# Kernel optimization log

Measured on AMD Instinct MI355X. Metric: run time of the kernel, lower is better.

## Reference

```python
import jax, jax.numpy as jnp
import numpy as np

B, T, C = 2, 2048, 1024
H = 16
HS = C // H  # head_size = 64


def setup_inputs() -> dict:
    key = jax.random.key(0)
    k1, k2, k3 = jax.random.split(key, 3)
    x = jax.random.normal(k1, (B, T, C), dtype=jnp.float32)
    # nn.Linear(n_embd, 3*n_embd): weight [3C, C], bias [3C]
    W = jax.random.normal(k2, (3 * C, C), dtype=jnp.float32) * (C ** -0.5)
    b = jax.random.normal(k3, (3 * C,), dtype=jnp.float32) * 0.02
    return {"x": x, "W": W, "b": b}


def reference(x, W, b):
    Bs, Ts, Cs = x.shape
    # fused QKV projection: [B,T,3C]
    qkv = x @ W.T + b
    qkv = qkv.reshape(Bs, Ts, 3, H, HS)
    q, k, v = jnp.moveaxis(qkv, 2, 0)          # each [B,T,H,HS]
    q = q.transpose(0, 2, 1, 3)                 # [B,H,T,HS]
    k = k.transpose(0, 2, 1, 3)
    v = v.transpose(0, 2, 1, 3)
    scale = HS ** -0.5
    wei = jnp.einsum('bhqd,bhkd->bhqk', q, k) * scale  # [B,H,T,T]
    causal = jnp.tril(jnp.ones((Ts, Ts), dtype=bool))
    wei = jnp.where(causal, wei, -jnp.inf)
    wei = jax.nn.softmax(wei, axis=-1)
    out = jnp.einsum('bhqk,bhkd->bhqd', wei, v)        # [B,H,T,HS]
    return out.transpose(0, 2, 1, 3).reshape(Bs, Ts, Cs)
```

## Files before the change

### kernel.cpp

```cpp
#include <hip/hip_runtime.h>
#include <hip/hip_bf16.h>

typedef __attribute__((ext_vector_type(8))) short bf16x8;
typedef __attribute__((ext_vector_type(4))) float f32x4;

#define BATCH 2
#define T_SEQ 2048
#define C_EMB 1024
#define NH 16
#define HS 64

__device__ __forceinline__ void gld_lds16(const __hip_bfloat16* g, void* l) {
    __builtin_amdgcn_global_load_lds((const __attribute__((address_space(1))) uint32_t*)g,
                                     (__attribute__((address_space(3))) uint32_t*)l, 16, 0, 0);
}

__device__ __forceinline__ unsigned pk_bf16(float a, float b) {
    unsigned r;
    asm("v_cvt_pk_bf16_f32 %0, %1, %2" : "=v"(r) : "v"(a), "v"(b));
    return r;
}

__device__ __forceinline__ void pack_store(char* dst, float4 a, float4 b) {
    uint4 u;
    u.x = pk_bf16(a.x, a.y);
    u.y = pk_bf16(a.z, a.w);
    u.z = pk_bf16(b.x, b.y);
    u.w = pk_bf16(b.z, b.w);
    *(uint4*)dst = u;
}

#define NT_K 16

__launch_bounds__(512, 2)
__global__ void qkv_gemm(const float* __restrict__ xf,
                         const float* __restrict__ wf,
                         const float* __restrict__ bias,
                         __hip_bfloat16* __restrict__ qo,
                         __hip_bfloat16* __restrict__ ko,
                         __hip_bfloat16* __restrict__ vto)
{
    __shared__ __align__(16) char smem[114688];
    __hip_bfloat16* ASB = (__hip_bfloat16*)smem;
    __hip_bfloat16* BSB = (__hip_bfloat16*)(smem + 65536);
    const int nTn = (3 * C_EMB) / 192;
    int bid = blockIdx.x;
    int wgid = (bid & 7) * 32 + (bid >> 3);
    int bm = wgid / nTn, bn = wgid % nTn;
    int m0 = bm * 256, n0 = bn * 192;
    int tid  = threadIdx.x;
    int lane = tid & 63, w = tid >> 6;
    int wr = w >> 2, wc = w & 3;
    int c = lane & 15, g = lane >> 4;
    int sr = lane >> 2;
    int j  = lane & 3;
    int pc = j ^ ((sr >> 1) & 3);
    int rchnk = (g ^ ((c >> 1) & 3)) << 4;

#define LOAD_AB(kt, kh, pa_, pb_) { \
    int col_ = (kt) * 64 + (kh) * 32 + j * 8; \
    _Pragma("unroll") for (int i_ = 0; i_ < 2; ++i_) { \
        const float* s_ = &xf[(size_t)(m0 + w * 32 + i_ * 16 + sr) * 1024 + col_]; \
        pa_[2 * i_] = *(const float4*)s_; pa_[2 * i_ + 1] = *(const float4*)(s_ + 4); } \
    if (w < 4) { \
        _Pragma("unroll") for (int i_ = 0; i_ < 2; ++i_) { \
            const float* s_ = &wf[(size_t)(n0 + w * 32 + i_ * 16 + sr) * 1024 + col_]; \
            pb_[2 * i_] = *(const float4*)s_; pb_[2 * i_ + 1] = *(const float4*)(s_ + 4); } \
    } else { \
        const float* s_ = &wf[(size_t)(n0 + 128 + (w - 4) * 16 + sr) * 1024 + col_]; \
        pb_[0] = *(const float4*)s_; pb_[1] = *(const float4*)(s_ + 4); } }

#define WRITE_AB(tb_, pa_, pb_) { \
    _Pragma("unroll") for (int i_ = 0; i_ < 2; ++i_) \
        pack_store((char*)&ASB[(tb_) * 8192 + (w * 32 + i_ * 16 + sr) * 32 + pc * 8], \
                   pa_[2 * i_], pa_[2 * i_ + 1]); \
    if (w < 4) { \
        _Pragma("unroll") for (int i_ = 0; i_ < 2; ++i_) \
            pack_store((char*)&BSB[(tb_) * 6144 + (w * 32 + i_ * 16 + sr) * 32 + pc * 8], \
                       pb_[2 * i_], pb_[2 * i_ + 1]); \
    } else { \
        pack_store((char*)&BSB[(tb_) * 6144 + (128 + (w - 4) * 16 + sr) * 32 + pc * 8], \
                   pb_[0], pb_[1]); } }

    f32x4 acc[8][3];
#pragma unroll
    for (int mi = 0; mi < 8; ++mi)
#pragma unroll
        for (int ni = 0; ni < 3; ++ni)
            acc[mi][ni] = (f32x4){0.f, 0.f, 0.f, 0.f};

    float4 s0a[4], s0b[4], s1a[4], s1b[4];
    int tb_s0 = 0, tb_s1 = 0;
    bool v_s0 = false, v_s1 = false;

    LOAD_AB(0, 0, s0a, s0b); WRITE_AB(0, s0a, s0b);
    LOAD_AB(0, 1, s0a, s0b); WRITE_AB(1, s0a, s0b);
    LOAD_AB(1, 0, s1a, s1b); tb_s1 = 2; v_s1 = true;
    __syncthreads();

    for (int t = 0; t < NT_K; ++t) {
        int buf = t & 1;
#pragma unroll
        for (int ks = 0; ks < 2; ++ks) {
            const __hip_bfloat16* AL = &ASB[(buf * 2 + ks) * 8192];
            const __hip_bfloat16* BL = &BSB[(buf * 2 + ks) * 6144];
            bf16x8 bfr[3], af[8];
#pragma unroll
            for (int ni = 0; ni < 3; ++ni)
                bfr[ni] = *(const bf16x8*)((const char*)BL + (wc * 48 + ni * 16 + c) * 64 + rchnk);
#pragma unroll
            for (int mi = 0; mi < 8; ++mi)
                af[mi] = *(const bf16x8*)((const char*)AL + (wr * 128 + mi * 16 + c) * 64 + rchnk);
            if (ks == 0) {
                if (t + 1 < NT_K) { LOAD_AB(t + 1, 1, s0a, s0b); tb_s0 = ((t + 1) & 1) * 2 + 1; v_s0 = true; }
                else v_s0 = false;
            } else {
                if (t + 2 < NT_K) { LOAD_AB(t + 2, 0, s1a, s1b); tb_s1 = ((t + 2) & 1) * 2; v_s1 = true; }
                else v_s1 = false;
            }
            __builtin_amdgcn_s_setprio(1);
#pragma unroll
            for (int mi = 0; mi < 8; ++mi)
#pragma unroll
                for (int ni = 0; ni < 3; ++ni)
                    acc[mi][ni] = __builtin_amdgcn_mfma_f32_16x16x32_bf16(af[mi], bfr[ni], acc[mi][ni], 0, 0, 0);
            __builtin_amdgcn_s_setprio(0);
            if (ks == 0) { if (v_s1) WRITE_AB(tb_s1, s1a, s1b); }
            else         { if (v_s0) WRITE_AB(tb_s0, s0a, s0b); }
            asm volatile("s_waitcnt lgkmcnt(0)" ::: "memory");
            __builtin_amdgcn_s_barrier();
        }
    }
#undef LOAD_AB
#undef WRITE_AB

    const float QSCALE = 0.125f * 1.44269504088896340736f;
    __syncthreads();
    int b = m0 >> 11;
    int t0 = (m0 & (T_SEQ - 1)) + wr * 128;
#pragma unroll
    for (int ni = 0; ni < 3; ++ni) {
        int nb = n0 + wc * 48 + ni * 16;
        int s = nb >> 10;
        int h = (nb >> 6) & (NH - 1);
        float bv = bias[nb + c];
        if (s < 2) {
            __hip_bfloat16* dst = (s == 0) ? qo : ko;
            float scale = (s == 0) ? QSCALE : 1.0f;
            int dd = (nb & 63) + c;
            size_t bhb = (size_t)(b * NH + h) * T_SEQ;
#pragma unroll
            for (int mi = 0; mi < 8; ++mi) {
#pragma unroll
                for (int r = 0; r < 4; ++r) {
                    int tt = t0 + mi * 16 + g * 4 + r;
                    dst[(bhb + tt) * HS + dd] = __float2bfloat16((acc[mi][ni][r] + bv) * scale);
                }
            }
        } else {
            int dbase = nb & 63;
            char* scr = smem + (w * 3 + ni) * 4096;
#pragma unroll
            for (int mi = 0; mi < 8; ++mi) {
#pragma unroll
                for (int r = 0; r < 4; ++r) {
                    int m = mi * 16 + g * 4 + r;
                    __hip_bfloat16 hv = __float2bfloat16(acc[mi][ni][r] + bv);
                    *(ushort*)(scr + c * 256 + ((((m >> 3) ^ c) & 15) << 4) + (m & 7) * 2) = *(ushort*)&hv;
                }
            }
            size_t bh = (size_t)(b * NH + h);
#pragma unroll
            for (int p = 0; p < 4; ++p) {
                int d = p * 4 + g;
                bf16x8 vv = *(bf16x8*)(scr + d * 256 + (((c ^ d) & 15) << 4));
                *(bf16x8*)(&vto[(bh * HS + dbase + d) * T_SEQ + t0 + c * 8]) = vv;
            }
        }
    }
}

__launch_bounds__(256, 4)
__global__ void attn_fwd(const __hip_bfloat16* __restrict__ qb,
                         const __hip_bfloat16* __restrict__ kb,
                         const __hip_bfloat16* __restrict__ vtb,
                         float* __restrict__ out)
{
    __shared__ __align__(16) char smem[40960];

    int idx = blockIdx.x;
    int bh = idx & 31;
    int qt = 31 - (idx >> 5);
    int w  = threadIdx.x >> 6;
    int lane = threadIdx.x & 63;
    int c = lane & 15, g = lane >> 4;
    char* p_strip = smem + 32768 + w * 2048;

    const __hip_bfloat16* Qp = qb  + (size_t)bh * T_SEQ * HS;
    const __hip_bfloat16* Kp = kb  + (size_t)bh * T_SEQ * HS;
    const __hip_bfloat16* Vp = vtb + (size_t)bh * HS * T_SEQ;
    int b = bh >> 4, h = bh & (NH - 1);

    int srow = lane >> 3;
    int scol = ((lane & 7) ^ srow) << 3;
    int swz  = (c & 7) << 4;
    int krow0 = w * 16 + srow;
    int krow1 = w * 16 + 8 + srow;
    int qw = qt * 64 + w * 16;
    int ntile = qt + 1;

    bf16x8 qf[2];
    qf[0] = *(const bf16x8*)(&Qp[(size_t)(qw + c) * HS + g * 8]);
    qf[1] = *(const bf16x8*)(&Qp[(size_t)(qw + c) * HS + 32 + g * 8]);

    f32x4 oacc[4];
#pragma unroll
    for (int i = 0; i < 4; ++i) oacc[i] = (f32x4){0.f, 0.f, 0.f, 0.f};
    float lrow = 0.f;

#define ATT_STAGE(t_, buf_) { \
    int k0_ = (t_) * 64; \
    char* kb_ = smem + (buf_) * 8192; \
    char* vb_ = smem + 16384 + (buf_) * 8192; \
    gld_lds16(&Kp[(size_t)(k0_ + krow0) * HS + scol],  kb_ + (w * 16) * 128); \
    gld_lds16(&Kp[(size_t)(k0_ + krow1) * HS + scol],  kb_ + (w * 16 + 8) * 128); \
    gld_lds16(&Vp[(size_t)krow0 * T_SEQ + k0_ + scol], vb_ + (w * 16) * 128); \
    gld_lds16(&Vp[(size_t)krow1 * T_SEQ + k0_ + scol], vb_ + (w * 16 + 8) * 128); }

    ATT_STAGE(0, 0);

    for (int tix = 0; tix < ntile; ++tix) {
        int cur = tix & 1;
        asm volatile("s_waitcnt vmcnt(0)" ::: "memory");
        __builtin_amdgcn_s_barrier();
        if (tix + 1 < ntile) ATT_STAGE(tix + 1, cur ^ 1);

        bool diag = (tix == ntile - 1);
        const char* KL = smem + cur * 8192;
        const char* VL = smem + 16384 + cur * 8192;

        f32x4 sacc[4];
#pragma unroll
        for (int i = 0; i < 4; ++i) sacc[i] = (f32x4){0.f, 0.f, 0.f, 0.f};
        __builtin_amdgcn_s_setprio(1);
#pragma unroll
        for (int ks = 0; ks < 2; ++ks)
#pragma unroll
            for (int kc = 0; kc < 4; ++kc)
                if (!diag || kc <= w) {
                    int rr = kc * 16 + c;
                    int colB = (ks * 64 + g * 16) ^ swz;
                    bf16x8 kf = *(const bf16x8*)(KL + rr * 128 + colB);
                    sacc[kc] = __builtin_amdgcn_mfma_f32_16x16x32_bf16(kf, qf[ks], sacc[kc], 0, 0, 0);
                }
        __builtin_amdgcn_s_setprio(0);

#pragma unroll
        for (int kc = 0; kc < 4; ++kc) {
            float p0, p1, p2, p3;
            if (!diag) {
                p0 = __builtin_amdgcn_exp2f(sacc[kc][0]);
                p1 = __builtin_amdgcn_exp2f(sacc[kc][1]);
                p2 = __builtin_amdgcn_exp2f(sacc[kc][2]);
                p3 = __builtin_amdgcn_exp2f(sacc[kc][3]);
            } else {
                int kbase = kc * 16 + g * 4;
                int lim = w * 16 + c;
                p0 = (kc <= w && kbase + 0 <= lim) ? __builtin_amdgcn_exp2f(sacc[kc][0]) : 0.f;
                p1 = (kc <= w && kbase + 1 <= lim) ? __builtin_amdgcn_exp2f(sacc[kc][1]) : 0.f;
                p2 = (kc <= w && kbase + 2 <= lim) ? __builtin_amdgcn_exp2f(sacc[kc][2]) : 0.f;
                p3 = (kc <= w && kbase + 3 <= lim) ? __builtin_amdgcn_exp2f(sacc[kc][3]) : 0.f;
            }
            lrow += (p0 + p1) + (p2 + p3);
            unsigned lo = pk_bf16(p0, p1);
            unsigned hi = pk_bf16(p2, p3);
            int gran = ((kc * 2 + (g >> 1)) ^ (c & 7)) << 4;
            *(uint2*)(p_strip + c * 128 + gran + ((g & 1) << 3)) = make_uint2(lo, hi);
        }

        int ksm = diag ? ((w >= 2) ? 2 : 1) : 2;
        __builtin_amdgcn_s_setprio(1);
#pragma unroll
        for (int ks = 0; ks < 2; ++ks) {
            if (ks >= ksm) break;
            int pgran = ((ks * 4 + g) ^ (c & 7)) << 4;
            bf16x8 pf = *(bf16x8*)(p_strip + c * 128 + pgran);
#pragma unroll
            for (int d16 = 0; d16 < 4; ++d16) {
                int dr = d16 * 16 + c;
                int colB = (ks * 64 + g * 16) ^ swz;
                bf16x8 vf = *(const bf16x8*)(VL + dr * 128 + colB);
                oacc[d16] = __builtin_amdgcn_mfma_f32_16x16x32_bf16(vf, pf, oacc[d16], 0, 0, 0);
            }
        }
        __builtin_amdgcn_s_setprio(0);
    }

    float v = lrow;
    v += __shfl_xor(v, 16, 64);
    v += __shfl_xor(v, 32, 64);
    float linv = 1.0f / v;
    float* orow = &out[((size_t)(b * T_SEQ + qw + c)) * C_EMB + h * HS + g * 4];
#pragma unroll
    for (int d16 = 0; d16 < 4; ++d16) {
        float4 st;
        st.x = oacc[d16][0] * linv;
        st.y = oacc[d16][1] * linv;
        st.z = oacc[d16][2] * linv;
        st.w = oacc[d16][3] * linv;
        *(float4*)(&orow[d16 * 16]) = st;
    }
#undef ATT_STAGE
}

extern "C" void kernel_launch(void* const* d_in, const int* in_sizes, int n_in,
                              void* d_out, int out_size, void* d_ws, size_t ws_size,
                              hipStream_t stream) {
    const float* x    = (const float*)d_in[0];
    const float* W    = (const float*)d_in[1];
    const float* bias = (const float*)d_in[2];
    float* out = (float*)d_out;

    char* ws = (char*)d_ws;
    __hip_bfloat16* qo  = (__hip_bfloat16*)(ws + (14u << 20));
    __hip_bfloat16* ko  = (__hip_bfloat16*)(ws + (22u << 20));
    __hip_bfloat16* vto = (__hip_bfloat16*)(ws + (30u << 20));

    int gemm_grid = (BATCH * T_SEQ / 256) * (3 * C_EMB / 192);
    qkv_gemm<<<gemm_grid, 512, 0, stream>>>(x, W, bias, qo, ko, vto);

    attn_fwd<<<1024, 256, 0, stream>>>(qo, ko, vto, out);
}
```

Measured before the change: 74.14 us.

## Pre-convert W to bf16 and stream B tiles via global_load_lds

Adds a separate kernel that converts the fp32 weight matrix to bf16 in workspace every call. The QKV GEMM then loads B tiles directly into LDS with async global_load_lds, using vmcnt waits in place of register staging and pack-stores. The aim is to halve B-operand global traffic and free registers and VALU work inside the GEMM main loop. The cost is an extra kernel launch plus a full read and write pass over W, and the explicit vmcnt counts must match the number of outstanding loads.

```diff
diff --git a/kernel.cpp b/kernel.cpp
--- a/kernel.cpp
+++ b/kernel.cpp
@@ -30,11 +30,24 @@
     *(uint4*)dst = u;
 }
 
+__global__ void cvt_w(const float4* __restrict__ s, ushort4* __restrict__ d, int n4) {
+    int i = blockIdx.x * blockDim.x + threadIdx.x;
+    if (i >= n4) return;
+    float4 v = s[i];
+    ushort4 o;
+    __hip_bfloat16 h;
+    h = __float2bfloat16(v.x); o.x = *(ushort*)&h;
+    h = __float2bfloat16(v.y); o.y = *(ushort*)&h;
+    h = __float2bfloat16(v.z); o.z = *(ushort*)&h;
+    h = __float2bfloat16(v.w); o.w = *(ushort*)&h;
+    d[i] = o;
+}
+
 #define NT_K 16
 
 __launch_bounds__(512, 2)
 __global__ void qkv_gemm(const float* __restrict__ xf,
-                         const float* __restrict__ wf,
+                         const __hip_bfloat16* __restrict__ wb,
                          const float* __restrict__ bias,
                          __hip_bfloat16* __restrict__ qo,
                          __hip_bfloat16* __restrict__ ko,
@@ -55,32 +68,33 @@
     int sr = lane >> 2;
     int j  = lane & 3;
     int pc = j ^ ((sr >> 1) & 3);
+    int sj = j ^ ((sr >> 1) & 3);
     int rchnk = (g ^ ((c >> 1) & 3)) << 4;
 
-#define LOAD_AB(kt, kh, pa_, pb_) { \
+#define STAGE_B(kt, kh, buf) \
+    { if (w < 4) { \
+        gld_lds16(&wb[(size_t)(n0 + w * 32 + sr) * 1024 + (kt) * 64 + (kh) * 32 + sj * 8], \
+                  &BSB[((buf) * 2 + (kh)) * 6144 + (w * 32) * 32]); \
+        gld_lds16(&wb[(size_t)(n0 + w * 32 + 16 + sr) * 1024 + (kt) * 64 + (kh) * 32 + sj * 8], \
+                  &BSB[((buf) * 2 + (kh)) * 6144 + (w * 32 + 16) * 32]); \
+      } else { \
+        gld_lds16(&wb[(size_t)(n0 + 128 + (w - 4) * 16 + sr) * 1024 + (kt) * 64 + (kh) * 32 + sj * 8], \
+                  &BSB[((buf) * 2 + (kh)) * 6144 + (128 + (w - 4) * 16) * 32]); \
+      } }
+
+#define LOAD_A(kt, kh, pa_) { \
     int col_ = (kt) * 64 + (kh) * 32 + j * 8; \
     _Pragma("unroll") for (int i_ = 0; i_ < 2; ++i_) { \
         const float* s_ = &xf[(size_t)(m0 + w * 32 + i_ * 16 + sr) * 1024 + col_]; \
-        pa_[2 * i_] = *(const float4*)s_; pa_[2 * i_ + 1] = *(const float4*)(s_ + 4); } \
-    if (w < 4) { \
-        _Pragma("unroll") for (int i_ = 0; i_ < 2; ++i_) { \
-            const float* s_ = &wf[(size_t)(n0 + w * 32 + i_ * 16 + sr) * 1024 + col_]; \
-            pb_[2 * i_] = *(const float4*)s_; pb_[2 * i_ + 1] = *(const float4*)(s_ + 4); } \
-    } else { \
-        const float* s_ = &wf[(size_t)(n0 + 128 + (w - 4) * 16 + sr) * 1024 + col_]; \
-        pb_[0] = *(const float4*)s_; pb_[1] = *(const float4*)(s_ + 4); } }
-
-#define WRITE_AB(tb_, pa_, pb_) { \
+        pa_[2 * i_] = *(const float4*)s_; pa_[2 * i_ + 1] = *(const float4*)(s_ + 4); } }
+
+#define WRITE_A(tb_, pa_) { \
     _Pragma("unroll") for (int i_ = 0; i_ < 2; ++i_) \
         pack_store((char*)&ASB[(tb_) * 8192 + (w * 32 + i_ * 16 + sr) * 32 + pc * 8], \
-                   pa_[2 * i_], pa_[2 * i_ + 1]); \
-    if (w < 4) { \
-        _Pragma("unroll") for (int i_ = 0; i_ < 2; ++i_) \
-            pack_store((char*)&BSB[(tb_) * 6144 + (w * 32 + i_ * 16 + sr) * 32 + pc * 8], \
-                       pb_[2 * i_], pb_[2 * i_ + 1]); \
-    } else { \
-        pack_store((char*)&BSB[(tb_) * 6144 + (128 + (w - 4) * 16 + sr) * 32 + pc * 8], \
-                   pb_[0], pb_[1]); } }
+                   pa_[2 * i_], pa_[2 * i_ + 1]); }
+
+#define WAIT_STEADY() { if (w < 4) asm volatile("s_waitcnt vmcnt(10)" ::: "memory"); \
+                        else       asm volatile("s_waitcnt vmcnt(9)" ::: "memory"); }
 
     f32x4 acc[8][3];
 #pragma unroll
@@ -89,14 +103,16 @@
         for (int ni = 0; ni < 3; ++ni)
             acc[mi][ni] = (f32x4){0.f, 0.f, 0.f, 0.f};
 
-    float4 s0a[4], s0b[4], s1a[4], s1b[4];
+    float4 s0a[4], s1a[4];
     int tb_s0 = 0, tb_s1 = 0;
     bool v_s0 = false, v_s1 = false;
 
-    LOAD_AB(0, 0, s0a, s0b); WRITE_AB(0, s0a, s0b);
-    LOAD_AB(0, 1, s0a, s0b); WRITE_AB(1, s0a, s0b);
-    LOAD_AB(1, 0, s1a, s1b); tb_s1 = 2; v_s1 = true;
-    __syncthreads();
+    STAGE_B(0, 0, 0); STAGE_B(0, 1, 0); STAGE_B(1, 0, 1);
+    LOAD_A(0, 0, s0a); WRITE_A(0, s0a);
+    LOAD_A(0, 1, s0a); WRITE_A(1, s0a);
+    LOAD_A(1, 0, s1a); tb_s1 = 2; v_s1 = true;
+    asm volatile("s_waitcnt lgkmcnt(0)" ::: "memory");
+    __builtin_amdgcn_s_barrier();
 
     for (int t = 0; t < NT_K; ++t) {
         int buf = t & 1;
@@ -111,12 +127,19 @@
 #pragma unroll
             for (int mi = 0; mi < 8; ++mi)
                 af[mi] = *(const bf16x8*)((const char*)AL + (wr * 128 + mi * 16 + c) * 64 + rchnk);
+            bool staged;
             if (ks == 0) {
-                if (t + 1 < NT_K) { LOAD_AB(t + 1, 1, s0a, s0b); tb_s0 = ((t + 1) & 1) * 2 + 1; v_s0 = true; }
-                else v_s0 = false;
+                staged = (t + 1 < NT_K);
+                if (staged) {
+                    STAGE_B(t + 1, 1, buf ^ 1);
+                    LOAD_A(t + 1, 1, s0a); tb_s0 = ((t + 1) & 1) * 2 + 1; v_s0 = true;
+                } else v_s0 = false;
             } else {
-                if (t + 2 < NT_K) { LOAD_AB(t + 2, 0, s1a, s1b); tb_s1 = ((t + 2) & 1) * 2; v_s1 = true; }
-                else v_s1 = false;
+                staged = (t + 2 < NT_K);
+                if (staged) {
+                    STAGE_B(t + 2, 0, buf);
+                    LOAD_A(t + 2, 0, s1a); tb_s1 = ((t + 2) & 1) * 2; v_s1 = true;
+                } else v_s1 = false;
             }
             __builtin_amdgcn_s_setprio(1);
 #pragma unroll
@@ -125,14 +148,18 @@
                 for (int ni = 0; ni < 3; ++ni)
                     acc[mi][ni] = __builtin_amdgcn_mfma_f32_16x16x32_bf16(af[mi], bfr[ni], acc[mi][ni], 0, 0, 0);
             __builtin_amdgcn_s_setprio(0);
-            if (ks == 0) { if (v_s1) WRITE_AB(tb_s1, s1a, s1b); }
-            else         { if (v_s0) WRITE_AB(tb_s0, s0a, s0b); }
+            if (ks == 0) { if (v_s1) WRITE_A(tb_s1, s1a); }
+            else         { if (v_s0) WRITE_A(tb_s0, s0a); }
+            if (staged) { WAIT_STEADY(); }
+            else        { asm volatile("s_waitcnt vmcnt(0)" ::: "memory"); }
             asm volatile("s_waitcnt lgkmcnt(0)" ::: "memory");
             __builtin_amdgcn_s_barrier();
         }
     }
-#undef LOAD_AB
-#undef WRITE_AB
+#undef STAGE_B
+#undef LOAD_A
+#undef WRITE_A
+#undef WAIT_STEADY
 
     const float QSCALE = 0.125f * 1.44269504088896340736f;
     __syncthreads();
@@ -322,12 +349,16 @@
     float* out = (float*)d_out;
 
     char* ws = (char*)d_ws;
+    __hip_bfloat16* wbf = (__hip_bfloat16*)(ws);
     __hip_bfloat16* qo  = (__hip_bfloat16*)(ws + (14u << 20));
     __hip_bfloat16* ko  = (__hip_bfloat16*)(ws + (22u << 20));
     __hip_bfloat16* vto = (__hip_bfloat16*)(ws + (30u << 20));
 
+    int n4w = 3 * C_EMB * C_EMB / 4;
+    cvt_w<<<(n4w + 255) / 256, 256, 0, stream>>>((const float4*)W, (ushort4*)wbf, n4w);
+
     int gemm_grid = (BATCH * T_SEQ / 256) * (3 * C_EMB / 192);
-    qkv_gemm<<<gemm_grid, 512, 0, stream>>>(x, W, bias, qo, ko, vto);
+    qkv_gemm<<<gemm_grid, 512, 0, stream>>>(x, wbf, bias, qo, ko, vto);
 
     attn_fwd<<<1024, 256, 0, stream>>>(qo, ko, vto, out);
 }
```

Result: slower. 80.03 us (+7.9%).
